# Optimization experiments

Hardware: AMD Instinct MI355X
Metric: run time of the kernel (lower is better)

## Reference

```python
import jax, jax.numpy as jnp
import numpy as np

FILTER_LENGTH = 1024
HOP_LENGTH = 512
CUTOFF = FILTER_LENGTH // 2 + 1  # 513


def _make_forward_basis():
    n = FILTER_LENGTH
    fb = np.fft.fft(np.eye(n))
    fb = np.vstack([np.real(fb[:CUTOFF, :]), np.imag(fb[:CUTOFF, :])]).astype(np.float32)  # [2*cutoff, n]
    # hann window, fftbins=True (periodic); win_length == filter_length so pad_center is a no-op
    win = (0.5 - 0.5 * np.cos(2.0 * np.pi * np.arange(n) / n)).astype(np.float32)
    return jnp.asarray(fb * win[None, :])


def setup_inputs() -> dict:
    key = jax.random.key(0)
    B, T = 8, 1048576
    input_data = jax.random.normal(key, (B, T), dtype=jnp.float32)
    return {
        "input_data": input_data,
        "forward_basis": _make_forward_basis(),  # [1026, 1024]
        "eps": jnp.float32(1e-9),
    }


def reference(input_data, forward_basis, eps):
    pad = FILTER_LENGTH // 2
    x = jnp.pad(input_data, ((0, 0), (pad, pad)), mode="reflect")  # [B, T + filter_length]
    n_frames = (x.shape[1] - FILTER_LENGTH) // HOP_LENGTH + 1
    # gather overlapping frames: [B, n_frames, filter_length]
    idx = jnp.arange(n_frames)[:, None] * HOP_LENGTH + jnp.arange(FILTER_LENGTH)[None, :]
    frames = x[:, idx]
    # DFT via dense matmul: [B, 2*cutoff, n_frames]
    ft = jnp.einsum("fk,bnk->bfn", forward_basis, frames)
    real, imag = ft[:, :CUTOFF, :], ft[:, CUTOFF:, :]
    return jnp.sqrt(real * real + imag * imag + eps)
```

## Files before the change

### kernel.cpp

```cpp
#include <hip/hip_runtime.h>

#define T_LEN   1048576
#define NPAD    1049600
#define NFRAMES 2049
#define BATCH   8
#define NJ      (BATCH * NFRAMES)
#define NSEG    2050
#define SMAX    (BATCH * NSEG - 1)
#define CUT     513
#define MROWS   1026
#define MPAD    1152
#define OUT_BF  (CUT * NFRAMES)
#define NJT     129
#define PAD_BLOCKS (BATCH * (NPAD / 8) / 256)

typedef __attribute__((ext_vector_type(8))) short bf16x8_t;
typedef __attribute__((ext_vector_type(4))) float f32x4_t;

static __device__ __forceinline__ ushort f2bf(float f) {
    union { float f; unsigned u; } a;
    a.f = f;
    unsigned r = a.u + 0x7fffu + ((a.u >> 16) & 1u);
    return (ushort)(r >> 16);
}

static __device__ __forceinline__ void gl_lds16(const ushort* g, ushort* s) {
    __builtin_amdgcn_global_load_lds(
        (__attribute__((address_space(1))) void*)g,
        (__attribute__((address_space(3))) void*)s,
        16, 0, 0);
}

__global__ void prep_kernel(const float* __restrict__ in, const float* __restrict__ fb,
                            ushort* __restrict__ xpad, ushort* __restrict__ A2) {
    const int tid = threadIdx.x;
    if (blockIdx.x < PAD_BLOCKS) {
        int g  = blockIdx.x * 256 + tid;
        int b  = g / (NPAD / 8);
        int c  = g - b * (NPAD / 8);
        int i0 = c * 8;
        const float* inb = in + (size_t)b * T_LEN;
        ushort o[8];
        if (i0 >= 512 && i0 + 7 < 512 + T_LEN) {
            const float4 v0 = *(const float4*)(inb + (i0 - 512));
            const float4 v1 = *(const float4*)(inb + (i0 - 512) + 4);
            o[0]=f2bf(v0.x); o[1]=f2bf(v0.y); o[2]=f2bf(v0.z); o[3]=f2bf(v0.w);
            o[4]=f2bf(v1.x); o[5]=f2bf(v1.y); o[6]=f2bf(v1.z); o[7]=f2bf(v1.w);
        } else {
            for (int t = 0; t < 8; ++t) {
                int i = i0 + t;
                int src = (i < 512) ? (512 - i)
                        : (i < 512 + T_LEN) ? (i - 512)
                        : (2 * T_LEN + 510 - i);
                o[t] = f2bf(inb[src]);
            }
        }
        *(ulonglong2*)(xpad + (size_t)b * NPAD + i0) = *(ulonglong2*)o;
    } else {
        int g  = (blockIdx.x - PAD_BLOCKS) * 256 + tid;
        int r  = g >> 8;
        int cq = (g & 255) * 4;
        ushort4 o;
        if (r < MROWS) {
            int f = r >> 1, h = r & 1;
            const float4 v = *(const float4*)(fb + (size_t)(f + h * CUT) * 1024 + cq);
            o = make_ushort4(f2bf(v.x), f2bf(v.y), f2bf(v.z), f2bf(v.w));
        } else {
            o = make_ushort4(0, 0, 0, 0);
        }
        *(ushort4*)(A2 + (size_t)r * 1024 + cq) = o;
    }
}

__global__ __launch_bounds__(256) void gemm_kernel(
        const ushort* __restrict__ A2, const ushort* __restrict__ xpad,
        float* __restrict__ out, const float* __restrict__ epsp) {
    __shared__ __align__(16) ushort ldsA0[128 * 64];
    __shared__ __align__(16) ushort ldsA1[128 * 64];
    __shared__ __align__(16) ushort ldsB [136 * 64];

    const int bid = blockIdx.x;
    const int jt  = (bid / 72) * 8 + (bid & 7);
    const int mt  = (bid >> 3) % 9;
    if (jt >= NJT) return;

    const int tid  = threadIdx.x;
    const int wave = tid >> 6, lane = tid & 63;
    const int quad = lane >> 4, l15 = lane & 15;
    const int m0 = mt * 128;
    const int j0 = jt * 128;
    const int wm = (wave >> 1) * 64;
    const int wj = (wave & 1) * 64;

    const int b0 = j0 / NFRAMES;
    const int S0 = j0 + b0;

    const int sr  = lane >> 3;
    const int sc8 = ((lane & 7) ^ sr) * 8;

    int aoff[4], boff[4], boffx = 0;
    for (int t = 0; t < 4; ++t) {
        const int r = (wave * 4 + t) * 8 + sr;
        aoff[t] = (m0 + r) * 1024 + sc8;
        int S = S0 + r; if (S > SMAX) S = SMAX;
        int bb = S / NSEG, ss = S - bb * NSEG;
        boff[t] = bb * NPAD + ss * 512 + sc8;
    }
    {
        int S = S0 + 128 + sr; if (S > SMAX) S = SMAX;
        int bb = S / NSEG, ss = S - bb * NSEG;
        boffx = bb * NPAD + ss * 512 + sc8;
    }

    int rowb[4];
    for (int jx = 0; jx < 4; ++jx) {
        const int j = j0 + wj + jx * 16 + l15;
        rowb[jx] = wj + jx * 16 + l15 + (j / NFRAMES - b0);
    }

    f32x4_t acc[4][4] = {};

    for (int kt = 0; kt < 8; ++kt) {
        const int k0 = kt * 64;
        __syncthreads();
        for (int t = 0; t < 4; ++t) {
            gl_lds16(A2 + aoff[t] + k0,        &ldsA0[(wave * 4 + t) * 512]);
            gl_lds16(A2 + aoff[t] + 512 + k0,  &ldsA1[(wave * 4 + t) * 512]);
            gl_lds16(xpad + boff[t] + k0,      &ldsB [(wave * 4 + t) * 512]);
        }
        if (wave == 0) gl_lds16(xpad + boffx + k0, &ldsB[16 * 512]);
        __syncthreads();
        for (int kk = 0; kk < 2; ++kk) {
            const int cb = kk * 4 + quad;
            bf16x8_t a0[4], a1[4], bf0[4], bf1[4];
            const int asw = (cb ^ (l15 & 7)) * 8;
            for (int i = 0; i < 4; ++i) {
                const int ro = (wm + i * 16 + l15) * 64;
                a0[i] = *(const bf16x8_t*)&ldsA0[ro + asw];
                a1[i] = *(const bf16x8_t*)&ldsA1[ro + asw];
            }
            for (int jx = 0; jx < 4; ++jx) {
                const int r0 = rowb[jx];
                const int r1 = r0 + 1;
                bf0[jx] = *(const bf16x8_t*)&ldsB[r0 * 64 + ((cb ^ (r0 & 7)) * 8)];
                bf1[jx] = *(const bf16x8_t*)&ldsB[r1 * 64 + ((cb ^ (r1 & 7)) * 8)];
            }
            for (int i = 0; i < 4; ++i)
                for (int jx = 0; jx < 4; ++jx) {
                    acc[i][jx] = __builtin_amdgcn_mfma_f32_16x16x32_bf16(
                        a0[i], bf0[jx], acc[i][jx], 0, 0, 0);
                    acc[i][jx] = __builtin_amdgcn_mfma_f32_16x16x32_bf16(
                        a1[i], bf1[jx], acc[i][jx], 0, 0, 0);
                }
        }
    }

    const float eps = *epsp;
    for (int tj = 0; tj < 4; ++tj) {
        const int j = j0 + wj + tj * 16 + l15;
        if (j >= NJ) continue;
        const int b = j / NFRAMES;
        const int n = j - b * NFRAMES;
        float* ob = out + (size_t)b * OUT_BF + n;
        for (int ti = 0; ti < 4; ++ti) {
            const int M  = m0 + wm + ti * 16 + quad * 4;
            const int f0 = M >> 1;
            f32x4_t a = acc[ti][tj];
            if (f0 < CUT)
                ob[(size_t)f0 * NFRAMES] = sqrtf(a.x * a.x + a.y * a.y + eps);
            if (f0 + 1 < CUT)
                ob[(size_t)(f0 + 1) * NFRAMES] = sqrtf(a.z * a.z + a.w * a.w + eps);
        }
    }
}

extern "C" void kernel_launch(void* const* d_in, const int* in_sizes, int n_in,
                              void* d_out, int out_size, void* d_ws, size_t ws_size,
                              hipStream_t stream) {
    const float* in   = (const float*)d_in[0];
    const float* fb   = (const float*)d_in[1];
    const float* epsp = (const float*)d_in[2];
    float* out = (float*)d_out;

    ushort* A2   = (ushort*)d_ws;
    ushort* xpad = (ushort*)((char*)d_ws + (size_t)MPAD * 1024 * 2);

    prep_kernel<<<dim3(PAD_BLOCKS + MPAD), dim3(256), 0, stream>>>(in, fb, xpad, A2);
    gemm_kernel<<<dim3(17 * 72), dim3(256), 0, stream>>>(A2, xpad, out, epsp);
}
```

Baseline: 125.0 us.

## Exploit DFT conjugate symmetry to halve basis rows via odd-sample sign flip

Uses the real-input DFT symmetry: frequency 512-f is obtained from frequency f by negating odd-indexed samples, so only 257 frequency bins (514 interleaved rows) of the basis are loaded and the second accumulator computes the mirrored bins with sign-flipped B fragments. This cuts A-matrix traffic and the number of M tiles, reducing grid size while keeping MFMA count similar per output. It doubles accumulator registers (launch_bounds 256,2 added), which risks register pressure and spills. The bf16 sign-flip trick relies on the pairing of odd elements within each 32-bit word.

```diff
diff --git a/kernel.cpp b/kernel.cpp
--- a/kernel.cpp
+++ b/kernel.cpp
@@ -8,14 +8,15 @@
 #define NSEG    2050
 #define SMAX    (BATCH * NSEG - 1)
 #define CUT     513
-#define MROWS   1026
-#define MPAD    1152
+#define MS_ROWS 514
+#define MS_PAD  640
 #define OUT_BF  (CUT * NFRAMES)
 #define NJT     129
 #define PAD_BLOCKS (BATCH * (NPAD / 8) / 256)
 
 typedef __attribute__((ext_vector_type(8))) short bf16x8_t;
 typedef __attribute__((ext_vector_type(4))) float f32x4_t;
+typedef __attribute__((ext_vector_type(4))) int   i32x4_t;
 
 static __device__ __forceinline__ ushort f2bf(float f) {
     union { float f; unsigned u; } a;
@@ -29,6 +30,15 @@
         (__attribute__((address_space(1))) void*)g,
         (__attribute__((address_space(3))) void*)s,
         16, 0, 0);
+}
+
+static __device__ __forceinline__ bf16x8_t oddflip(bf16x8_t v) {
+    i32x4_t w;
+    __builtin_memcpy(&w, &v, 16);
+    w.x ^= 0x80000000; w.y ^= 0x80000000; w.z ^= 0x80000000; w.w ^= 0x80000000;
+    bf16x8_t r;
+    __builtin_memcpy(&r, &w, 16);
+    return r;
 }
 
 __global__ void prep_kernel(const float* __restrict__ in, const float* __restrict__ fb,
@@ -61,7 +71,7 @@
         int r  = g >> 8;
         int cq = (g & 255) * 4;
         ushort4 o;
-        if (r < MROWS) {
+        if (r < MS_ROWS) {
             int f = r >> 1, h = r & 1;
             const float4 v = *(const float4*)(fb + (size_t)(f + h * CUT) * 1024 + cq);
             o = make_ushort4(f2bf(v.x), f2bf(v.y), f2bf(v.z), f2bf(v.w));
@@ -72,7 +82,7 @@
     }
 }
 
-__global__ __launch_bounds__(256) void gemm_kernel(
+__global__ __launch_bounds__(256, 2) void gemm_kernel(
         const ushort* __restrict__ A2, const ushort* __restrict__ xpad,
         float* __restrict__ out, const float* __restrict__ epsp) {
     __shared__ __align__(16) ushort ldsA0[128 * 64];
@@ -80,8 +90,8 @@
     __shared__ __align__(16) ushort ldsB [136 * 64];
 
     const int bid = blockIdx.x;
-    const int jt  = (bid / 72) * 8 + (bid & 7);
-    const int mt  = (bid >> 3) % 9;
+    const int jt  = (bid / 40) * 8 + (bid & 7);
+    const int mt  = (bid >> 3) % 5;
     if (jt >= NJT) return;
 
     const int tid  = threadIdx.x;
@@ -118,7 +128,8 @@
         rowb[jx] = wj + jx * 16 + l15 + (j / NFRAMES - b0);
     }
 
-    f32x4_t acc[4][4] = {};
+    f32x4_t acc1[4][4] = {};
+    f32x4_t acc2[4][4] = {};
 
     for (int kt = 0; kt < 8; ++kt) {
         const int k0 = kt * 64;
@@ -147,10 +158,21 @@
             }
             for (int i = 0; i < 4; ++i)
                 for (int jx = 0; jx < 4; ++jx) {
-                    acc[i][jx] = __builtin_amdgcn_mfma_f32_16x16x32_bf16(
-                        a0[i], bf0[jx], acc[i][jx], 0, 0, 0);
-                    acc[i][jx] = __builtin_amdgcn_mfma_f32_16x16x32_bf16(
-                        a1[i], bf1[jx], acc[i][jx], 0, 0, 0);
+                    acc1[i][jx] = __builtin_amdgcn_mfma_f32_16x16x32_bf16(
+                        a0[i], bf0[jx], acc1[i][jx], 0, 0, 0);
+                    acc1[i][jx] = __builtin_amdgcn_mfma_f32_16x16x32_bf16(
+                        a1[i], bf1[jx], acc1[i][jx], 0, 0, 0);
+                }
+            for (int jx = 0; jx < 4; ++jx) {
+                bf0[jx] = oddflip(bf0[jx]);
+                bf1[jx] = oddflip(bf1[jx]);
+            }
+            for (int i = 0; i < 4; ++i)
+                for (int jx = 0; jx < 4; ++jx) {
+                    acc2[i][jx] = __builtin_amdgcn_mfma_f32_16x16x32_bf16(
+                        a0[i], bf0[jx], acc2[i][jx], 0, 0, 0);
+                    acc2[i][jx] = __builtin_amdgcn_mfma_f32_16x16x32_bf16(
+                        a1[i], bf1[jx], acc2[i][jx], 0, 0, 0);
                 }
         }
     }
@@ -165,11 +187,20 @@
         for (int ti = 0; ti < 4; ++ti) {
             const int M  = m0 + wm + ti * 16 + quad * 4;
             const int f0 = M >> 1;
-            f32x4_t a = acc[ti][tj];
-            if (f0 < CUT)
-                ob[(size_t)f0 * NFRAMES] = sqrtf(a.x * a.x + a.y * a.y + eps);
-            if (f0 + 1 < CUT)
-                ob[(size_t)(f0 + 1) * NFRAMES] = sqrtf(a.z * a.z + a.w * a.w + eps);
+            f32x4_t c1 = acc1[ti][tj];
+            f32x4_t c2 = acc2[ti][tj];
+            if (f0 <= 256) {
+                ob[(size_t)f0 * NFRAMES] =
+                    sqrtf(c1.x * c1.x + c1.y * c1.y + eps);
+                ob[(size_t)(512 - f0) * NFRAMES] =
+                    sqrtf(c2.x * c2.x + c2.y * c2.y + eps);
+            }
+            if (f0 + 1 <= 256) {
+                ob[(size_t)(f0 + 1) * NFRAMES] =
+                    sqrtf(c1.z * c1.z + c1.w * c1.w + eps);
+                ob[(size_t)(511 - f0) * NFRAMES] =
+                    sqrtf(c2.z * c2.z + c2.w * c2.w + eps);
+            }
         }
     }
 }
@@ -183,8 +214,8 @@
     float* out = (float*)d_out;
 
     ushort* A2   = (ushort*)d_ws;
-    ushort* xpad = (ushort*)((char*)d_ws + (size_t)MPAD * 1024 * 2);
-
-    prep_kernel<<<dim3(PAD_BLOCKS + MPAD), dim3(256), 0, stream>>>(in, fb, xpad, A2);
-    gemm_kernel<<<dim3(17 * 72), dim3(256), 0, stream>>>(A2, xpad, out, epsp);
-}
+    ushort* xpad = (ushort*)((char*)d_ws + (size_t)MS_PAD * 1024 * 2);
+
+    prep_kernel<<<dim3(PAD_BLOCKS + MS_PAD), dim3(256), 0, stream>>>(in, fb, xpad, A2);
+    gemm_kernel<<<dim3(17 * 40), dim3(256), 0, stream>>>(A2, xpad, out, epsp);
+}
```

After: 132.4 us. 1.06x slower.
